# Kernel tuning notes

Measured on AMD Instinct MI355X. Metric: run time of the kernel, lower is better.

The kernel has to match this reference:

```python
import jax, jax.numpy as jnp
import numpy as np

N = 100000  # nodes
E = 1600000  # edges

def gcn_layer(x, W, b, src, tgt, ew):
    # support = x @ W + b ; messages gathered at src, weighted scatter-sum into tgt
    h = x @ W + b                      # [N, F_out]
    msg = h[src] * ew[:, None]         # [E, F_out]
    return jax.ops.segment_sum(msg, tgt, num_segments=N)  # [N, F_out]

def setup_inputs() -> dict:
    key = jax.random.key(0)
    ks = jax.random.split(key, 12)
    nfeat, nhid, nclass = 256, 128, 40
    x = jax.random.normal(ks[0], (N, nfeat), dtype=jnp.float32)
    src = jax.random.randint(ks[1], (E,), 0, N)
    tgt = jax.random.randint(ks[2], (E,), 0, N)
    edge_weight = jax.random.uniform(ks[3], (E,), dtype=jnp.float32)
    def w(k, fi, fo):
        return jax.random.normal(k, (fi, fo), dtype=jnp.float32) / np.sqrt(fi)
    return {
        "x": x, "src": src, "tgt": tgt, "edge_weight": edge_weight,
        "W0": w(ks[4], nfeat, nhid), "b0": jnp.zeros((nhid,), jnp.float32),
        "W1": w(ks[5], nhid, nhid),  "b1": jnp.zeros((nhid,), jnp.float32),
        "W2": w(ks[6], nhid, nhid),  "b2": jnp.zeros((nhid,), jnp.float32),
        "W3": w(ks[7], nhid, nclass),"b3": jnp.zeros((nclass,), jnp.float32),
    }

def reference(x, src, tgt, edge_weight, W0, b0, W1, b1, W2, b2, W3, b3):
    # RESK2 with nlayers=4, eval mode (dropout = identity).
    # x0 = relu(gc0); r = x0; x1 = relu(gc1); x2 = relu(gc2) + r; out = log_softmax(gc3)
    x0 = jax.nn.relu(gcn_layer(x, W0, b0, src, tgt, edge_weight))
    r = x0
    x1 = jax.nn.relu(gcn_layer(x0, W1, b1, src, tgt, edge_weight))
    x2 = jax.nn.relu(gcn_layer(x1, W2, b2, src, tgt, edge_weight)) + r
    logits = gcn_layer(x2, W3, b3, src, tgt, edge_weight)
    return jax.nn.log_softmax(logits, axis=1)
```

## Files before the change

kernel.cpp:

```cpp
#include <hip/hip_runtime.h>
#include <hip/hip_bf16.h>


typedef __attribute__((ext_vector_type(8))) short short8;
typedef __attribute__((ext_vector_type(4))) float float4v;

#define SC_SHIFT 8
#define SC_NODES 256
#define FILL_CAP 12288
#define SRC_MASK 0x1FFFF

static __device__ __forceinline__ float bf2f_lo(unsigned int v) {
    return __uint_as_float(v << 16);
}
static __device__ __forceinline__ float bf2f_hi(unsigned int v) {
    return __uint_as_float(v & 0xffff0000u);
}
static __device__ __forceinline__ unsigned short f2bf(float f) {
    unsigned int u = __float_as_uint(f);
    u = (u + 0x7fffu + ((u >> 16) & 1u)) >> 16;
    return (unsigned short)u;
}
static __device__ __forceinline__ unsigned int packbf(float a, float b) {
    return (unsigned int)f2bf(a) | ((unsigned int)f2bf(b) << 16);
}
static __device__ __forceinline__ float pw_w(unsigned int pe) {
    return __uint_as_float((pe >> 17) << 16);
}

static __device__ __forceinline__ void acc8(float* acc, uint4 v, float wt) {
    acc[0] = fmaf(bf2f_lo(v.x), wt, acc[0]);
    acc[1] = fmaf(bf2f_hi(v.x), wt, acc[1]);
    acc[2] = fmaf(bf2f_lo(v.y), wt, acc[2]);
    acc[3] = fmaf(bf2f_hi(v.y), wt, acc[3]);
    acc[4] = fmaf(bf2f_lo(v.z), wt, acc[4]);
    acc[5] = fmaf(bf2f_hi(v.z), wt, acc[5]);
    acc[6] = fmaf(bf2f_lo(v.w), wt, acc[6]);
    acc[7] = fmaf(bf2f_hi(v.w), wt, acc[7]);
}
static __device__ __forceinline__ void acc4(float* acc, uint2 v, float wt) {
    acc[0] = fmaf(bf2f_lo(v.x), wt, acc[0]);
    acc[1] = fmaf(bf2f_hi(v.x), wt, acc[1]);
    acc[2] = fmaf(bf2f_lo(v.y), wt, acc[2]);
    acc[3] = fmaf(bf2f_hi(v.y), wt, acc[3]);
}

__global__ __launch_bounds__(256) void k_count(const int* __restrict__ tgt,
                                               int* __restrict__ chunkTot,
                                               int E, int NSC) {
    __shared__ int hist[512];
    const int tid = threadIdx.x;
    hist[tid] = 0;
    hist[tid + 256] = 0;
    __syncthreads();
#pragma unroll
    for (int r = 0; r < 4; r++) {
        int e = blockIdx.x * 4096 + r * 1024 + tid * 4;
        if (e + 3 < E) {
            int4 tv = *(const int4*)&tgt[e];
            atomicAdd(&hist[tv.x >> SC_SHIFT], 1);
            atomicAdd(&hist[tv.y >> SC_SHIFT], 1);
            atomicAdd(&hist[tv.z >> SC_SHIFT], 1);
            atomicAdd(&hist[tv.w >> SC_SHIFT], 1);
        } else {
            for (int j = 0; j < 4; j++)
                if (e + j < E) atomicAdd(&hist[tgt[e + j] >> SC_SHIFT], 1);
        }
    }
    __syncthreads();
    for (int i = tid; i < NSC; i += 256) {
        int c = hist[i];
        if (c) atomicAdd(&chunkTot[i], c);
    }
}

__global__ __launch_bounds__(512) void k_scanB(const int* __restrict__ chunkTot,
                                               int* __restrict__ chunkStart,
                                               int* __restrict__ chunkCur,
                                               int E, int NSC) {
    __shared__ int sm[512];
    const int tid = threadIdx.x;
    int v = (tid < NSC) ? chunkTot[tid] : 0;
    sm[tid] = v;
    __syncthreads();
    for (int off = 1; off < 512; off <<= 1) {
        int t = (tid >= off) ? sm[tid - off] : 0;
        __syncthreads();
        sm[tid] += t;
        __syncthreads();
    }
    int excl = sm[tid] - v;
    if (tid < NSC) {
        chunkStart[tid] = excl;
        chunkCur[tid * 32] = excl;
    }
    if (tid == 0) chunkStart[NSC] = E;
}

__global__ __launch_bounds__(512) void k_bucket(const int* __restrict__ src,
                                                const int* __restrict__ tgt,
                                                const float* __restrict__ ew,
                                                int* __restrict__ chunkCur,
                                                unsigned int* __restrict__ st_pw,
                                                unsigned char* __restrict__ st_t8,
                                                int E) {
    __shared__ int cnt[512];
    __shared__ int rk[512];
    __shared__ int bbase[512];
    const int tid = threadIdx.x;
    cnt[tid] = 0;
    rk[tid] = 0;
    __syncthreads();

    int t16[16];
    unsigned int p16[16];
#pragma unroll
    for (int r = 0; r < 4; r++) {
        int e = blockIdx.x * 8192 + r * 2048 + tid * 4;
        if (e + 3 < E) {
            int4 tv = *(const int4*)&tgt[e];
            int4 sv = *(const int4*)&src[e];
            float4 wv = *(const float4*)&ew[e];
            t16[r * 4 + 0] = tv.x; t16[r * 4 + 1] = tv.y;
            t16[r * 4 + 2] = tv.z; t16[r * 4 + 3] = tv.w;
            p16[r * 4 + 0] = ((unsigned int)f2bf(wv.x) << 17) | (unsigned int)sv.x;
            p16[r * 4 + 1] = ((unsigned int)f2bf(wv.y) << 17) | (unsigned int)sv.y;
            p16[r * 4 + 2] = ((unsigned int)f2bf(wv.z) << 17) | (unsigned int)sv.z;
            p16[r * 4 + 3] = ((unsigned int)f2bf(wv.w) << 17) | (unsigned int)sv.w;
        } else {
            for (int j = 0; j < 4; j++) {
                int ee = e + j;
                t16[r * 4 + j] = (ee < E) ? tgt[ee] : -1;
                p16[r * 4 + j] = (ee < E)
                    ? (((unsigned int)f2bf(ew[ee]) << 17) | (unsigned int)src[ee])
                    : 0u;
            }
        }
    }
#pragma unroll
    for (int j = 0; j < 16; j++)
        if (t16[j] >= 0) atomicAdd(&cnt[t16[j] >> SC_SHIFT], 1);
    __syncthreads();
    {
        int c = cnt[tid];
        bbase[tid] = c ? atomicAdd(&chunkCur[tid * 32], c) : 0;
    }
    __syncthreads();
#pragma unroll
    for (int j = 0; j < 16; j++) {
        if (t16[j] >= 0) {
            int c = t16[j] >> SC_SHIFT;
            int pos = bbase[c] + atomicAdd(&rk[c], 1);
            st_pw[pos] = p16[j];
            st_t8[pos] = (unsigned char)(t16[j] & (SC_NODES - 1));
        }
    }
}

__global__ __launch_bounds__(256) void k_fill2(const unsigned int* __restrict__ st_pw,
                                               const unsigned char* __restrict__ st_t8,
                                               const int* __restrict__ chunkStart,
                                               int* __restrict__ rowptr,
                                               unsigned int* __restrict__ perm,
                                               int N, int E, int NSC) {
    __shared__ int lhist[SC_NODES];
    __shared__ int lcur[SC_NODES];
    __shared__ unsigned int ledge[FILL_CAP];
    const int tid = threadIdx.x;
    const int b = blockIdx.x;
    const int n0 = b << SC_SHIFT;
    const int nlocal = min(SC_NODES, N - n0);
    const int sstart = chunkStart[b];
    const int send = chunkStart[b + 1];
    const int cnt = send - sstart;

    lhist[tid] = 0;
    __syncthreads();
    for (int e = sstart + tid; e < send; e += 256)
        atomicAdd(&lhist[st_t8[e]], 1);
    __syncthreads();
    int v = lhist[tid];
    __syncthreads();
    lhist[tid] = v;
    __syncthreads();
    for (int off = 1; off < 256; off <<= 1) {
        int t = (tid >= off) ? lhist[tid - off] : 0;
        __syncthreads();
        lhist[tid] += t;
        __syncthreads();
    }
    int excl = lhist[tid] - v;
    if (tid < nlocal) rowptr[n0 + tid] = sstart + excl;
    if (b == NSC - 1 && tid == 0) rowptr[N] = E;
    lcur[tid] = excl;
    __syncthreads();

    if (cnt <= FILL_CAP) {
        for (int e = sstart + tid; e < send; e += 256) {
            int lt = st_t8[e];
            int pos = atomicAdd(&lcur[lt], 1);
            ledge[pos] = st_pw[e];
        }
        __syncthreads();
        for (int i = tid; i < cnt; i += 256) perm[sstart + i] = ledge[i];
    } else {
        for (int e = sstart + tid; e < send; e += 256) {
            int lt = st_t8[e];
            int pos = atomicAdd(&lcur[lt], 1);
            perm[sstart + pos] = st_pw[e];
        }
    }
}

__global__ __launch_bounds__(256) void k_wtrans_all(
    const float* __restrict__ W0, const float* __restrict__ W1,
    const float* __restrict__ W2, const float* __restrict__ W3,
    unsigned short* __restrict__ Wt0, unsigned short* __restrict__ Wt1,
    unsigned short* __restrict__ Wt2, unsigned short* __restrict__ Wt3,
    int* __restrict__ chunkTot) {
    int idx = blockIdx.x * 256 + threadIdx.x;
    if (idx < 512) chunkTot[idx] = 0;
    if (idx < 32768) {
        int c = idx >> 8, k = idx & 255;
        Wt0[idx] = f2bf(W0[k * 128 + c]);
    } else if (idx < 49152) {
        int i = idx - 32768;
        int c = i >> 7, k = i & 127;
        Wt1[i] = f2bf(W1[k * 128 + c]);
    } else if (idx < 65536) {
        int i = idx - 49152;
        int c = i >> 7, k = i & 127;
        Wt2[i] = f2bf(W2[k * 128 + c]);
    } else if (idx < 71680) {
        int i = idx - 65536;
        int c = i >> 7, k = i & 127;
        Wt3[i] = (c < 40) ? f2bf(W3[k * 40 + c]) : 0;
    }
}

template <int K, int AF32>
__global__ __launch_bounds__(256) void k_gemm_mfma(const void* __restrict__ Av,
                                                   const unsigned short* __restrict__ Wt,
                                                   const float* __restrict__ bias,
                                                   unsigned short* __restrict__ C, int N) {
    __shared__ union {
        struct {
            unsigned short As[64 * 40];
            unsigned short Bs[128 * 40];
        } s;
        unsigned short Cs[64 * 136];
    } u;
    __shared__ float bsh[128];
    const unsigned short* A16 = (const unsigned short*)Av;
    const float* A32 = (const float*)Av;
    const int tid = threadIdx.x;
    const int wave = tid >> 6, lane = tid & 63;
    const int quad = lane >> 4, l15 = lane & 15;
    const int rowBase = blockIdx.x * 64;

    if (tid < 128) bsh[tid] = bias[tid];

    const int r0 = tid >> 2, kc0 = tid & 3;
    const int rB1 = r0, rB2 = r0 + 64;
    int rg0 = rowBase + r0;
    rg0 = rg0 < N ? rg0 : N - 1;

    uint4 pa, pb0, pb1;
    auto load_step = [&](int k0) {
        if (AF32) {
            float4 f0 = *(const float4*)&A32[(size_t)rg0 * K + k0 + kc0 * 8];
            float4 f1 = *(const float4*)&A32[(size_t)rg0 * K + k0 + kc0 * 8 + 4];
            pa.x = packbf(f0.x, f0.y);
            pa.y = packbf(f0.z, f0.w);
            pa.z = packbf(f1.x, f1.y);
            pa.w = packbf(f1.z, f1.w);
        } else {
            pa = *(const uint4*)&A16[(size_t)rg0 * K + k0 + kc0 * 8];
        }
        pb0 = *(const uint4*)&Wt[(size_t)rB1 * K + k0 + kc0 * 8];
        pb1 = *(const uint4*)&Wt[(size_t)rB2 * K + k0 + kc0 * 8];
    };

    const float4v z = {0.f, 0.f, 0.f, 0.f};
    float4v acc[8];
#pragma unroll
    for (int j = 0; j < 8; j++) acc[j] = z;

    load_step(0);
    for (int k0 = 0; k0 < K; k0 += 32) {
        *(uint4*)&u.s.As[r0 * 40 + kc0 * 8] = pa;
        *(uint4*)&u.s.Bs[rB1 * 40 + kc0 * 8] = pb0;
        *(uint4*)&u.s.Bs[rB2 * 40 + kc0 * 8] = pb1;
        __syncthreads();
        if (k0 + 32 < K) load_step(k0 + 32);

        short8 a = *(const short8*)&u.s.As[(wave * 16 + l15) * 40 + quad * 8];
#pragma unroll
        for (int c = 0; c < 8; c++) {
            short8 b = *(const short8*)&u.s.Bs[(c * 16 + l15) * 40 + quad * 8];
            acc[c] = __builtin_amdgcn_mfma_f32_16x16x32_bf16(b, a, acc[c], 0, 0, 0);
        }
        __syncthreads();
    }

#pragma unroll
    for (int c = 0; c < 8; c++) {
        int colBase = c * 16 + quad * 4;
        float4 bv = *(const float4*)&bsh[colBase];
        uint2 o;
        o.x = packbf(acc[c][0] + bv.x, acc[c][1] + bv.y);
        o.y = packbf(acc[c][2] + bv.z, acc[c][3] + bv.w);
        *(uint2*)&u.Cs[(wave * 16 + l15) * 136 + colBase] = o;
    }
    __syncthreads();
#pragma unroll
    for (int i = 0; i < 4; i++) {
        int flat = i * 256 + tid;
        int row = flat >> 4, q = flat & 15;
        int grow = rowBase + row;
        if (grow < N) {
            uint4 v = *(const uint4*)&u.Cs[row * 136 + q * 8];
            *(uint4*)&C[(size_t)grow * 128 + q * 8] = v;
        }
    }
}

__global__ __launch_bounds__(256) void k_gemm40_mfma(const unsigned short* __restrict__ A,
                                                     const unsigned short* __restrict__ Wt3,
                                                     const float* __restrict__ bias,
                                                     unsigned short* __restrict__ C, int N) {
    __shared__ union {
        struct {
            unsigned short As[64 * 40];
            unsigned short Bs[48 * 136];
        } s;
        unsigned short Cs[64 * 72];
    } u;
    __shared__ float bsh[64];
    const int tid = threadIdx.x;
    const int wave = tid >> 6, lane = tid & 63;
    const int quad = lane >> 4, l15 = lane & 15;
    const int rowBase = blockIdx.x * 64;

    if (tid < 64) bsh[tid] = (tid < 40) ? bias[tid] : 0.f;

    const int r0 = tid >> 2, kc0 = tid & 3;
    int rg0 = rowBase + r0;
    rg0 = rg0 < N ? rg0 : N - 1;

    for (int t = tid; t < 48 * 16; t += 256) {
        int r = t >> 4, kc = t & 15;
        uint4 v = *(const uint4*)&Wt3[r * 128 + kc * 8];
        *(uint4*)&u.s.Bs[r * 136 + kc * 8] = v;
    }

    uint4 pa;
    auto load_step = [&](int k0) {
        pa = *(const uint4*)&A[(size_t)rg0 * 128 + k0 + kc0 * 8];
    };

    const float4v z = {0.f, 0.f, 0.f, 0.f};
    float4v acc[3];
#pragma unroll
    for (int j = 0; j < 3; j++) acc[j] = z;

    load_step(0);
    for (int k0 = 0; k0 < 128; k0 += 32) {
        *(uint4*)&u.s.As[r0 * 40 + kc0 * 8] = pa;
        __syncthreads();
        if (k0 + 32 < 128) load_step(k0 + 32);

        short8 a = *(const short8*)&u.s.As[(wave * 16 + l15) * 40 + quad * 8];
#pragma unroll
        for (int c = 0; c < 3; c++) {
            short8 b = *(const short8*)&u.s.Bs[(c * 16 + l15) * 136 + k0 + quad * 8];
            acc[c] = __builtin_amdgcn_mfma_f32_16x16x32_bf16(b, a, acc[c], 0, 0, 0);
        }
        __syncthreads();
    }

#pragma unroll
    for (int c = 0; c < 4; c++) {
        int colBase = c * 16 + quad * 4;
        uint2 o;
        if (c < 3) {
            float4 bv = *(const float4*)&bsh[colBase];
            o.x = packbf(acc[c][0] + bv.x, acc[c][1] + bv.y);
            o.y = packbf(acc[c][2] + bv.z, acc[c][3] + bv.w);
        } else {
            o.x = 0u;
            o.y = 0u;
        }
        *(uint2*)&u.Cs[(wave * 16 + l15) * 72 + colBase] = o;
    }
    __syncthreads();
#pragma unroll
    for (int i = 0; i < 2; i++) {
        int flat = i * 256 + tid;
        int row = flat >> 3, q = flat & 7;
        int grow = rowBase + row;
        if (grow < N) {
            uint4 v = *(const uint4*)&u.Cs[row * 72 + q * 8];
            *(uint4*)&C[(size_t)grow * 64 + q * 8] = v;
        }
    }
}

__global__ __launch_bounds__(256) void k_agg128(const unsigned short* __restrict__ h,
                                                const int* __restrict__ rowptr,
                                                const unsigned int* __restrict__ perm,
                                                const unsigned short* __restrict__ resid,
                                                unsigned short* __restrict__ out, int N) {
    int node = (blockIdx.x * 256 + threadIdx.x) >> 6;
    if (node >= N) return;
    const int lane = threadIdx.x & 63;
    const int g = lane >> 4, l = lane & 15;
    const int beg = rowptr[node], end = rowptr[node + 1];
    const int last = end - 1;

    float acc[8] = {};
    for (int base = beg; base < end; base += 16) {
        int e0 = base + g, e1 = base + 4 + g, e2 = base + 8 + g, e3 = base + 12 + g;
        unsigned int p0 = perm[e0 <= last ? e0 : last];
        unsigned int p1 = perm[e1 <= last ? e1 : last];
        unsigned int p2 = perm[e2 <= last ? e2 : last];
        unsigned int p3 = perm[e3 <= last ? e3 : last];
        uint4 a0 = *(const uint4*)&h[(size_t)(p0 & SRC_MASK) * 128 + l * 8];
        uint4 a1 = *(const uint4*)&h[(size_t)(p1 & SRC_MASK) * 128 + l * 8];
        uint4 a2 = *(const uint4*)&h[(size_t)(p2 & SRC_MASK) * 128 + l * 8];
        uint4 a3 = *(const uint4*)&h[(size_t)(p3 & SRC_MASK) * 128 + l * 8];
        float w0 = e0 <= last ? pw_w(p0) : 0.f;
        float w1 = e1 <= last ? pw_w(p1) : 0.f;
        float w2 = e2 <= last ? pw_w(p2) : 0.f;
        float w3 = e3 <= last ? pw_w(p3) : 0.f;
        acc8(acc, a0, w0);
        acc8(acc, a1, w1);
        acc8(acc, a2, w2);
        acc8(acc, a3, w3);
    }

#pragma unroll
    for (int i = 0; i < 8; i++) {
        acc[i] += __shfl_xor(acc[i], 16);
        acc[i] += __shfl_xor(acc[i], 32);
    }

    if (g == 0) {
#pragma unroll
        for (int i = 0; i < 8; i++) acc[i] = fmaxf(acc[i], 0.f);
        if (resid) {
            uint4 rv = *(const uint4*)&resid[(size_t)node * 128 + l * 8];
            acc[0] += bf2f_lo(rv.x); acc[1] += bf2f_hi(rv.x);
            acc[2] += bf2f_lo(rv.y); acc[3] += bf2f_hi(rv.y);
            acc[4] += bf2f_lo(rv.z); acc[5] += bf2f_hi(rv.z);
            acc[6] += bf2f_lo(rv.w); acc[7] += bf2f_hi(rv.w);
        }
        uint4 o;
        o.x = packbf(acc[0], acc[1]);
        o.y = packbf(acc[2], acc[3]);
        o.z = packbf(acc[4], acc[5]);
        o.w = packbf(acc[6], acc[7]);
        *(uint4*)&out[(size_t)node * 128 + l * 8] = o;
    }
}

__global__ __launch_bounds__(256) void k_agg40_lsm(const unsigned short* __restrict__ h,
                                                   const int* __restrict__ rowptr,
                                                   const unsigned int* __restrict__ perm,
                                                   float* __restrict__ out, int N) {
    int node = (blockIdx.x * 256 + threadIdx.x) >> 6;
    if (node >= N) return;
    const int lane = threadIdx.x & 63;
    const int g = lane >> 4, l = lane & 15;
    const int beg = rowptr[node], end = rowptr[node + 1];
    const int last = end - 1;
    const int lc = l < 10 ? l : 0;

    float acc[4] = {};
    for (int base = beg; base < end; base += 16) {
        int e0 = base + g, e1 = base + 4 + g, e2 = base + 8 + g, e3 = base + 12 + g;
        unsigned int p0 = perm[e0 <= last ? e0 : last];
        unsigned int p1 = perm[e1 <= last ? e1 : last];
        unsigned int p2 = perm[e2 <= last ? e2 : last];
        unsigned int p3 = perm[e3 <= last ? e3 : last];
        uint2 a0 = *(const uint2*)&h[(size_t)(p0 & SRC_MASK) * 64 + lc * 4];
        uint2 a1 = *(const uint2*)&h[(size_t)(p1 & SRC_MASK) * 64 + lc * 4];
        uint2 a2 = *(const uint2*)&h[(size_t)(p2 & SRC_MASK) * 64 + lc * 4];
        uint2 a3 = *(const uint2*)&h[(size_t)(p3 & SRC_MASK) * 64 + lc * 4];
        float w0 = e0 <= last ? pw_w(p0) : 0.f;
        float w1 = e1 <= last ? pw_w(p1) : 0.f;
        float w2 = e2 <= last ? pw_w(p2) : 0.f;
        float w3 = e3 <= last ? pw_w(p3) : 0.f;
        acc4(acc, a0, w0);
        acc4(acc, a1, w1);
        acc4(acc, a2, w2);
        acc4(acc, a3, w3);
    }
#pragma unroll
    for (int i = 0; i < 4; i++) {
        acc[i] += __shfl_xor(acc[i], 16);
        acc[i] += __shfl_xor(acc[i], 32);
    }

    bool vf = l < 10;
    float m = vf ? fmaxf(fmaxf(acc[0], acc[1]), fmaxf(acc[2], acc[3]))
                 : -__builtin_inff();
#pragma unroll
    for (int off = 1; off < 16; off <<= 1) m = fmaxf(m, __shfl_xor(m, off));
    float s = vf ? (expf(acc[0] - m) + expf(acc[1] - m) +
                    expf(acc[2] - m) + expf(acc[3] - m))
                 : 0.f;
#pragma unroll
    for (int off = 1; off < 16; off <<= 1) s += __shfl_xor(s, off);
    float ls = m + logf(s);
    if (g == 0 && vf) {
        float4 o = make_float4(acc[0] - ls, acc[1] - ls, acc[2] - ls, acc[3] - ls);
        *(float4*)&out[(size_t)node * 40 + l * 4] = o;
    }
}

extern "C" void kernel_launch(void* const* d_in, const int* in_sizes, int n_in,
                              void* d_out, int out_size, void* d_ws, size_t ws_size,
                              hipStream_t stream) {
    const float* x  = (const float*)d_in[0];
    const int*   src = (const int*)d_in[1];
    const int*   tgt = (const int*)d_in[2];
    const float* ew  = (const float*)d_in[3];
    const float* W0 = (const float*)d_in[4];
    const float* b0 = (const float*)d_in[5];
    const float* W1 = (const float*)d_in[6];
    const float* b1 = (const float*)d_in[7];
    const float* W2 = (const float*)d_in[8];
    const float* b2 = (const float*)d_in[9];
    const float* W3 = (const float*)d_in[10];
    const float* b3 = (const float*)d_in[11];

    const int N = in_sizes[0] / 256;
    const int E = in_sizes[1];
    const int NSC = (N + SC_NODES - 1) >> SC_SHIFT;

    char* ws = (char*)d_ws;
    size_t off = 0;
    auto alloc = [&](size_t bytes) -> void* {
        void* p = ws + off;
        off = (off + bytes + 255) & ~(size_t)255;
        return p;
    };
    unsigned short* XCb = (unsigned short*)alloc((size_t)N * 128 * 2);
    size_t hbytes = (size_t)N * 128 * 2;
    size_t sbytes = (size_t)E * 5 + 256;
    char* hbuf = (char*)alloc(hbytes > sbytes ? hbytes : sbytes);
    unsigned short* Hb = (unsigned short*)hbuf;
    unsigned int* st_pw = (unsigned int*)hbuf;
    unsigned char* st_t8 = (unsigned char*)(hbuf + (size_t)E * 4);
    char* buf1 = (char*)alloc((size_t)N * 128 * 2);
    unsigned short* XAb  = (unsigned short*)buf1;
    unsigned short* H40b = (unsigned short*)buf1;
    unsigned short* XBb  = (unsigned short*)alloc((size_t)N * 128 * 2);
    int*   rowptr    = (int*)alloc((size_t)(N + 1) * 4);
    int*   chunkTot  = (int*)alloc(512 * 4);
    int*   chunkStart= (int*)alloc(520 * 4);
    int*   chunkCur  = (int*)alloc(512 * 32 * 4);
    unsigned int* perm = (unsigned int*)alloc((size_t)E * 4);
    unsigned short* Wt0 = (unsigned short*)alloc(256 * 128 * 2);
    unsigned short* Wt1 = (unsigned short*)alloc(128 * 128 * 2);
    unsigned short* Wt2 = (unsigned short*)alloc(128 * 128 * 2);
    unsigned short* Wt3 = (unsigned short*)alloc(48 * 128 * 2);
    (void)ws_size;

    float* logits = (float*)d_out;

    k_wtrans_all<<<(71680 + 255) / 256, 256, 0, stream>>>(W0, W1, W2, W3,
                                                          Wt0, Wt1, Wt2, Wt3,
                                                          chunkTot);
    k_count<<<(E + 4095) / 4096, 256, 0, stream>>>(tgt, chunkTot, E, NSC);
    k_scanB<<<1, 512, 0, stream>>>(chunkTot, chunkStart, chunkCur, E, NSC);
    k_bucket<<<(E + 8191) / 8192, 512, 0, stream>>>(src, tgt, ew, chunkCur,
                                                    st_pw, st_t8, E);
    k_fill2<<<NSC, 256, 0, stream>>>(st_pw, st_t8, chunkStart, rowptr, perm,
                                     N, E, NSC);

    const int gGemm = (N + 63) / 64;
    const int gWave = (N + 3) / 4;

    k_gemm_mfma<256, 1><<<gGemm, 256, 0, stream>>>(x, Wt0, b0, Hb, N);
    k_agg128<<<gWave, 256, 0, stream>>>(Hb, rowptr, perm, nullptr, XAb, N);
    k_gemm_mfma<128, 0><<<gGemm, 256, 0, stream>>>(XAb, Wt1, b1, Hb, N);
    k_agg128<<<gWave, 256, 0, stream>>>(Hb, rowptr, perm, nullptr, XBb, N);
    k_gemm_mfma<128, 0><<<gGemm, 256, 0, stream>>>(XBb, Wt2, b2, Hb, N);
    k_agg128<<<gWave, 256, 0, stream>>>(Hb, rowptr, perm, XAb, XCb, N);
    k_gemm40_mfma<<<gGemm, 256, 0, stream>>>(XCb, Wt3, b3, H40b, N);
    k_agg40_lsm<<<gWave, 256, 0, stream>>>(H40b, rowptr, perm, logits, N);
}
```

Baseline: 490.8 us.

## Double GEMM row tile, compact layer-3 output rows, and peel aggregation tails

The MFMA GEMMs now compute 128 rows per block instead of 64, with each wave doing two 16-row tiles so each B fragment is reused twice and grid size halves. The 40-column GEMM writes compact 40-element (80-byte) rows instead of 64-padded ones, which shrinks the gathered data in the final aggregation. Both aggregation kernels split the edge loop into an unguarded full-16 body and a guarded tail, and use byte-offset address arithmetic. The cost is more LDS and accumulator registers per block, which may lower occupancy.

```diff
diff --git a/kernel.cpp b/kernel.cpp
--- a/kernel.cpp
+++ b/kernel.cpp
@@ -245,10 +245,10 @@
                                                    unsigned short* __restrict__ C, int N) {
     __shared__ union {
         struct {
-            unsigned short As[64 * 40];
+            unsigned short As[128 * 40];
             unsigned short Bs[128 * 40];
         } s;
-        unsigned short Cs[64 * 136];
+        unsigned short Cs[128 * 136];
     } u;
     __shared__ float bsh[128];
     const unsigned short* A16 = (const unsigned short*)Av;
@@ -256,49 +256,57 @@
     const int tid = threadIdx.x;
     const int wave = tid >> 6, lane = tid & 63;
     const int quad = lane >> 4, l15 = lane & 15;
-    const int rowBase = blockIdx.x * 64;
+    const int rowBase = blockIdx.x * 128;
 
     if (tid < 128) bsh[tid] = bias[tid];
 
-    const int r0 = tid >> 2, kc0 = tid & 3;
-    const int rB1 = r0, rB2 = r0 + 64;
+    const int r0 = tid >> 1, kh = (tid & 1) * 16;
     int rg0 = rowBase + r0;
     rg0 = rg0 < N ? rg0 : N - 1;
 
-    uint4 pa, pb0, pb1;
+    uint4 pa0, pa1, pb0, pb1;
     auto load_step = [&](int k0) {
         if (AF32) {
-            float4 f0 = *(const float4*)&A32[(size_t)rg0 * K + k0 + kc0 * 8];
-            float4 f1 = *(const float4*)&A32[(size_t)rg0 * K + k0 + kc0 * 8 + 4];
-            pa.x = packbf(f0.x, f0.y);
-            pa.y = packbf(f0.z, f0.w);
-            pa.z = packbf(f1.x, f1.y);
-            pa.w = packbf(f1.z, f1.w);
+            const float* ap = &A32[(size_t)rg0 * K + k0 + kh];
+            float4 f0 = *(const float4*)&ap[0];
+            float4 f1 = *(const float4*)&ap[4];
+            float4 f2 = *(const float4*)&ap[8];
+            float4 f3 = *(const float4*)&ap[12];
+            pa0.x = packbf(f0.x, f0.y); pa0.y = packbf(f0.z, f0.w);
+            pa0.z = packbf(f1.x, f1.y); pa0.w = packbf(f1.z, f1.w);
+            pa1.x = packbf(f2.x, f2.y); pa1.y = packbf(f2.z, f2.w);
+            pa1.z = packbf(f3.x, f3.y); pa1.w = packbf(f3.z, f3.w);
         } else {
-            pa = *(const uint4*)&A16[(size_t)rg0 * K + k0 + kc0 * 8];
-        }
-        pb0 = *(const uint4*)&Wt[(size_t)rB1 * K + k0 + kc0 * 8];
-        pb1 = *(const uint4*)&Wt[(size_t)rB2 * K + k0 + kc0 * 8];
+            const unsigned short* ap = &A16[(size_t)rg0 * K + k0 + kh];
+            pa0 = *(const uint4*)&ap[0];
+            pa1 = *(const uint4*)&ap[8];
+        }
+        const unsigned short* bp = &Wt[(size_t)r0 * K + k0 + kh];
+        pb0 = *(const uint4*)&bp[0];
+        pb1 = *(const uint4*)&bp[8];
     };
 
     const float4v z = {0.f, 0.f, 0.f, 0.f};
-    float4v acc[8];
-#pragma unroll
-    for (int j = 0; j < 8; j++) acc[j] = z;
+    float4v acc0[8], acc1[8];
+#pragma unroll
+    for (int j = 0; j < 8; j++) { acc0[j] = z; acc1[j] = z; }
 
     load_step(0);
     for (int k0 = 0; k0 < K; k0 += 32) {
-        *(uint4*)&u.s.As[r0 * 40 + kc0 * 8] = pa;
-        *(uint4*)&u.s.Bs[rB1 * 40 + kc0 * 8] = pb0;
-        *(uint4*)&u.s.Bs[rB2 * 40 + kc0 * 8] = pb1;
+        *(uint4*)&u.s.As[r0 * 40 + kh] = pa0;
+        *(uint4*)&u.s.As[r0 * 40 + kh + 8] = pa1;
+        *(uint4*)&u.s.Bs[r0 * 40 + kh] = pb0;
+        *(uint4*)&u.s.Bs[r0 * 40 + kh + 8] = pb1;
         __syncthreads();
         if (k0 + 32 < K) load_step(k0 + 32);
 
-        short8 a = *(const short8*)&u.s.As[(wave * 16 + l15) * 40 + quad * 8];
+        short8 a0 = *(const short8*)&u.s.As[(wave * 32 + l15) * 40 + quad * 8];
+        short8 a1 = *(const short8*)&u.s.As[(wave * 32 + 16 + l15) * 40 + quad * 8];
 #pragma unroll
         for (int c = 0; c < 8; c++) {
             short8 b = *(const short8*)&u.s.Bs[(c * 16 + l15) * 40 + quad * 8];
-            acc[c] = __builtin_amdgcn_mfma_f32_16x16x32_bf16(b, a, acc[c], 0, 0, 0);
+            acc0[c] = __builtin_amdgcn_mfma_f32_16x16x32_bf16(b, a0, acc0[c], 0, 0, 0);
+            acc1[c] = __builtin_amdgcn_mfma_f32_16x16x32_bf16(b, a1, acc1[c], 0, 0, 0);
         }
         __syncthreads();
     }
@@ -307,14 +315,17 @@
     for (int c = 0; c < 8; c++) {
         int colBase = c * 16 + quad * 4;
         float4 bv = *(const float4*)&bsh[colBase];
-        uint2 o;
-        o.x = packbf(acc[c][0] + bv.x, acc[c][1] + bv.y);
-        o.y = packbf(acc[c][2] + bv.z, acc[c][3] + bv.w);
-        *(uint2*)&u.Cs[(wave * 16 + l15) * 136 + colBase] = o;
-    }
-    __syncthreads();
-#pragma unroll
-    for (int i = 0; i < 4; i++) {
+        uint2 o0, o1;
+        o0.x = packbf(acc0[c][0] + bv.x, acc0[c][1] + bv.y);
+        o0.y = packbf(acc0[c][2] + bv.z, acc0[c][3] + bv.w);
+        o1.x = packbf(acc1[c][0] + bv.x, acc1[c][1] + bv.y);
+        o1.y = packbf(acc1[c][2] + bv.z, acc1[c][3] + bv.w);
+        *(uint2*)&u.Cs[(wave * 32 + l15) * 136 + colBase] = o0;
+        *(uint2*)&u.Cs[(wave * 32 + 16 + l15) * 136 + colBase] = o1;
+    }
+    __syncthreads();
+#pragma unroll
+    for (int i = 0; i < 8; i++) {
         int flat = i * 256 + tid;
         int row = flat >> 4, q = flat & 15;
         int grow = rowBase + row;
@@ -331,20 +342,20 @@
                                                      unsigned short* __restrict__ C, int N) {
     __shared__ union {
         struct {
-            unsigned short As[64 * 40];
+            unsigned short As[128 * 40];
             unsigned short Bs[48 * 136];
         } s;
-        unsigned short Cs[64 * 72];
+        unsigned short Cs[128 * 40];
     } u;
-    __shared__ float bsh[64];
+    __shared__ float bsh[48];
     const int tid = threadIdx.x;
     const int wave = tid >> 6, lane = tid & 63;
     const int quad = lane >> 4, l15 = lane & 15;
-    const int rowBase = blockIdx.x * 64;
-
-    if (tid < 64) bsh[tid] = (tid < 40) ? bias[tid] : 0.f;
-
-    const int r0 = tid >> 2, kc0 = tid & 3;
+    const int rowBase = blockIdx.x * 128;
+
+    if (tid < 48) bsh[tid] = (tid < 40) ? bias[tid] : 0.f;
+
+    const int r0 = tid >> 1, kh = (tid & 1) * 16;
     int rg0 = rowBase + r0;
     rg0 = rg0 < N ? rg0 : N - 1;
 
@@ -354,54 +365,61 @@
         *(uint4*)&u.s.Bs[r * 136 + kc * 8] = v;
     }
 
-    uint4 pa;
+    uint4 pa0, pa1;
     auto load_step = [&](int k0) {
-        pa = *(const uint4*)&A[(size_t)rg0 * 128 + k0 + kc0 * 8];
+        const unsigned short* ap = &A[(size_t)rg0 * 128 + k0 + kh];
+        pa0 = *(const uint4*)&ap[0];
+        pa1 = *(const uint4*)&ap[8];
     };
 
     const float4v z = {0.f, 0.f, 0.f, 0.f};
-    float4v acc[3];
-#pragma unroll
-    for (int j = 0; j < 3; j++) acc[j] = z;
+    float4v acc0[3], acc1[3];
+#pragma unroll
+    for (int j = 0; j < 3; j++) { acc0[j] = z; acc1[j] = z; }
 
     load_step(0);
     for (int k0 = 0; k0 < 128; k0 += 32) {
-        *(uint4*)&u.s.As[r0 * 40 + kc0 * 8] = pa;
+        *(uint4*)&u.s.As[r0 * 40 + kh] = pa0;
+        *(uint4*)&u.s.As[r0 * 40 + kh + 8] = pa1;
         __syncthreads();
         if (k0 + 32 < 128) load_step(k0 + 32);
 
-        short8 a = *(const short8*)&u.s.As[(wave * 16 + l15) * 40 + quad * 8];
+        short8 a0 = *(const short8*)&u.s.As[(wave * 32 + l15) * 40 + quad * 8];
+        short8 a1 = *(const short8*)&u.s.As[(wave * 32 + 16 + l15) * 40 + quad * 8];
 #pragma unroll
         for (int c = 0; c < 3; c++) {
             short8 b = *(const short8*)&u.s.Bs[(c * 16 + l15) * 136 + k0 + quad * 8];
-            acc[c] = __builtin_amdgcn_mfma_f32_16x16x32_bf16(b, a, acc[c], 0, 0, 0);
-        }
-        __syncthreads();
-    }
-
-#pragma unroll
-    for (int c = 0; c < 4; c++) {
+            acc0[c] = __builtin_amdgcn_mfma_f32_16x16x32_bf16(b, a0, acc0[c], 0, 0, 0);
+            acc1[c] = __builtin_amdgcn_mfma_f32_16x16x32_bf16(b, a1, acc1[c], 0, 0, 0);
+        }
+        __syncthreads();
+    }
+
+#pragma unroll
+    for (int c = 0; c < 3; c++) {
         int colBase = c * 16 + quad * 4;
-        uint2 o;
-        if (c < 3) {
+        if (c < 2 || quad < 2) {
             float4 bv = *(const float4*)&bsh[colBase];
-            o.x = packbf(acc[c][0] + bv.x, acc[c][1] + bv.y);
-            o.y = packbf(acc[c][2] + bv.z, acc[c][3] + bv.w);
-        } else {
-            o.x = 0u;
-            o.y = 0u;
-        }
-        *(uint2*)&u.Cs[(wave * 16 + l15) * 72 + colBase] = o;
-    }
-    __syncthreads();
-#pragma unroll
-    for (int i = 0; i < 2; i++) {
+            uint2 o0, o1;
+            o0.x = packbf(acc0[c][0] + bv.x, acc0[c][1] + bv.y);
+            o0.y = packbf(acc0[c][2] + bv.z, acc0[c][3] + bv.w);
+            o1.x = packbf(acc1[c][0] + bv.x, acc1[c][1] + bv.y);
+            o1.y = packbf(acc1[c][2] + bv.z, acc1[c][3] + bv.w);
+            *(uint2*)&u.Cs[(wave * 32 + l15) * 40 + colBase] = o0;
+            *(uint2*)&u.Cs[(wave * 32 + 16 + l15) * 40 + colBase] = o1;
+        }
+    }
+    __syncthreads();
+#pragma unroll
+    for (int i = 0; i < 3; i++) {
         int flat = i * 256 + tid;
-        int row = flat >> 3, q = flat & 7;
-        int grow = rowBase + row;
-        if (grow < N) {
-            uint4 v = *(const uint4*)&u.Cs[row * 72 + q * 8];
-            *(uint4*)&C[(size_t)grow * 64 + q * 8] = v;
+        if (flat < 640) {
+            int row = flat / 5, q = flat - row * 5;
+            int grow = rowBase + row;
+            if (grow < N) {
+                uint4 v = *(const uint4*)&u.Cs[row * 40 + q * 8];
+                *(uint4*)&C[(size_t)grow * 40 + q * 8] = v;
+            }
         }
     }
 }
@@ -416,27 +434,40 @@
     const int lane = threadIdx.x & 63;
     const int g = lane >> 4, l = lane & 15;
     const int beg = rowptr[node], end = rowptr[node + 1];
-    const int last = end - 1;
+    const char* hB = (const char*)h;
+    const unsigned int loff = (unsigned int)l * 16u;
 
     float acc[8] = {};
-    for (int base = beg; base < end; base += 16) {
-        int e0 = base + g, e1 = base + 4 + g, e2 = base + 8 + g, e3 = base + 12 + g;
-        unsigned int p0 = perm[e0 <= last ? e0 : last];
-        unsigned int p1 = perm[e1 <= last ? e1 : last];
-        unsigned int p2 = perm[e2 <= last ? e2 : last];
-        unsigned int p3 = perm[e3 <= last ? e3 : last];
-        uint4 a0 = *(const uint4*)&h[(size_t)(p0 & SRC_MASK) * 128 + l * 8];
-        uint4 a1 = *(const uint4*)&h[(size_t)(p1 & SRC_MASK) * 128 + l * 8];
-        uint4 a2 = *(const uint4*)&h[(size_t)(p2 & SRC_MASK) * 128 + l * 8];
-        uint4 a3 = *(const uint4*)&h[(size_t)(p3 & SRC_MASK) * 128 + l * 8];
-        float w0 = e0 <= last ? pw_w(p0) : 0.f;
-        float w1 = e1 <= last ? pw_w(p1) : 0.f;
-        float w2 = e2 <= last ? pw_w(p2) : 0.f;
-        float w3 = e3 <= last ? pw_w(p3) : 0.f;
-        acc8(acc, a0, w0);
-        acc8(acc, a1, w1);
-        acc8(acc, a2, w2);
-        acc8(acc, a3, w3);
+
+    int base = beg;
+    for (; base + 16 <= end; base += 16) {
+        unsigned int p0 = perm[base + g];
+        unsigned int p1 = perm[base + g + 4];
+        unsigned int p2 = perm[base + g + 8];
+        unsigned int p3 = perm[base + g + 12];
+        uint4 a0 = *(const uint4*)(hB + ((((p0 & SRC_MASK) << 8)) | loff));
+        uint4 a1 = *(const uint4*)(hB + ((((p1 & SRC_MASK) << 8)) | loff));
+        uint4 a2 = *(const uint4*)(hB + ((((p2 & SRC_MASK) << 8)) | loff));
+        uint4 a3 = *(const uint4*)(hB + ((((p3 & SRC_MASK) << 8)) | loff));
+        acc8(acc, a0, pw_w(p0));
+        acc8(acc, a1, pw_w(p1));
+        acc8(acc, a2, pw_w(p2));
+        acc8(acc, a3, pw_w(p3));
+    }
+    const int rem = end - base;
+    if (rem > 0) {
+        const int last = end - 1;
+        auto step = [&](int b4) {
+            int e = b4 + g;
+            unsigned int p = perm[e <= last ? e : last];
+            uint4 a = *(const uint4*)(hB + ((((p & SRC_MASK) << 8)) | loff));
+            float w = e <= last ? pw_w(p) : 0.f;
+            acc8(acc, a, w);
+        };
+        step(base);
+        if (rem > 4) step(base + 4);
+        if (rem > 8) step(base + 8);
+        if (rem > 12) step(base + 12);
     }
 
 #pragma unroll
@@ -473,28 +504,41 @@
     const int lane = threadIdx.x & 63;
     const int g = lane >> 4, l = lane & 15;
     const int beg = rowptr[node], end = rowptr[node + 1];
-    const int last = end - 1;
     const int lc = l < 10 ? l : 0;
+    const char* hB = (const char*)h;
+    const unsigned int loff = (unsigned int)lc * 8u;
 
     float acc[4] = {};
-    for (int base = beg; base < end; base += 16) {
-        int e0 = base + g, e1 = base + 4 + g, e2 = base + 8 + g, e3 = base + 12 + g;
-        unsigned int p0 = perm[e0 <= last ? e0 : last];
-        unsigned int p1 = perm[e1 <= last ? e1 : last];
-        unsigned int p2 = perm[e2 <= last ? e2 : last];
-        unsigned int p3 = perm[e3 <= last ? e3 : last];
-        uint2 a0 = *(const uint2*)&h[(size_t)(p0 & SRC_MASK) * 64 + lc * 4];
-        uint2 a1 = *(const uint2*)&h[(size_t)(p1 & SRC_MASK) * 64 + lc * 4];
-        uint2 a2 = *(const uint2*)&h[(size_t)(p2 & SRC_MASK) * 64 + lc * 4];
-        uint2 a3 = *(const uint2*)&h[(size_t)(p3 & SRC_MASK) * 64 + lc * 4];
-        float w0 = e0 <= last ? pw_w(p0) : 0.f;
-        float w1 = e1 <= last ? pw_w(p1) : 0.f;
-        float w2 = e2 <= last ? pw_w(p2) : 0.f;
-        float w3 = e3 <= last ? pw_w(p3) : 0.f;
-        acc4(acc, a0, w0);
-        acc4(acc, a1, w1);
-        acc4(acc, a2, w2);
-        acc4(acc, a3, w3);
+
+    int base = beg;
+    for (; base + 16 <= end; base += 16) {
+        unsigned int p0 = perm[base + g];
+        unsigned int p1 = perm[base + g + 4];
+        unsigned int p2 = perm[base + g + 8];
+        unsigned int p3 = perm[base + g + 12];
+        uint2 a0 = *(const uint2*)(hB + ((p0 & SRC_MASK) * 80u + loff));
+        uint2 a1 = *(const uint2*)(hB + ((p1 & SRC_MASK) * 80u + loff));
+        uint2 a2 = *(const uint2*)(hB + ((p2 & SRC_MASK) * 80u + loff));
+        uint2 a3 = *(const uint2*)(hB + ((p3 & SRC_MASK) * 80u + loff));
+        acc4(acc, a0, pw_w(p0));
+        acc4(acc, a1, pw_w(p1));
+        acc4(acc, a2, pw_w(p2));
+        acc4(acc, a3, pw_w(p3));
+    }
+    const int rem = end - base;
+    if (rem > 0) {
+        const int last = end - 1;
+        auto step = [&](int b4) {
+            int e = b4 + g;
+            unsigned int p = perm[e <= last ? e : last];
+            uint2 a = *(const uint2*)(hB + ((p & SRC_MASK) * 80u + loff));
+            float w = e <= last ? pw_w(p) : 0.f;
+            acc4(acc, a, w);
+        };
+        step(base);
+        if (rem > 4) step(base + 4);
+        if (rem > 8) step(base + 8);
+        if (rem > 12) step(base + 12);
     }
 #pragma unroll
     for (int i = 0; i < 4; i++) {
@@ -580,7 +624,7 @@
     k_fill2<<<NSC, 256, 0, stream>>>(st_pw, st_t8, chunkStart, rowptr, perm,
                                      N, E, NSC);
 
-    const int gGemm = (N + 63) / 64;
+    const int gGemm = (N + 127) / 128;
     const int gWave = (N + 3) / 4;
 
     k_gemm_mfma<256, 1><<<gGemm, 256, 0, stream>>>(x, Wt0, b0, Hb, N);
```

Measured after the change: 513.1 us. 4.5% more time.
